# Kernel tuning notes

Hardware: AMD Instinct MI355X
Metric: run time of the kernel (lower is better)

Reference implementation:

```python
import jax, jax.numpy as jnp
import numpy as np

N, E, D_IN, D_H, G = 20000, 320000, 512, 256, 128


def setup_inputs() -> dict:
    key = jax.random.key(0)
    ks = jax.random.split(key, 9)
    x = jax.random.normal(ks[0], (N, D_IN), dtype=jnp.float32)
    edge_index = jax.random.randint(ks[1], (2, E), 0, N, dtype=jnp.int32)
    batch = jnp.sort(jax.random.randint(ks[2], (N,), 0, G, dtype=jnp.int32))
    W1 = jax.random.normal(ks[3], (D_IN, D_H), dtype=jnp.float32) / np.float32(np.sqrt(D_IN))
    b1 = jnp.zeros((D_H,), dtype=jnp.float32)
    W2 = jax.random.normal(ks[4], (D_H, D_H), dtype=jnp.float32) / np.float32(np.sqrt(D_H))
    b2 = jnp.zeros((D_H,), dtype=jnp.float32)
    w_fc = jax.random.normal(ks[5], (D_H, 1), dtype=jnp.float32) / np.float32(np.sqrt(D_H))
    b_fc = jnp.zeros((1,), dtype=jnp.float32)
    return {"x": x, "edge_index": edge_index, "batch": batch,
            "W1": W1, "b1": b1, "W2": W2, "b2": b2, "w_fc": w_fc, "b_fc": b_fc}


def gcn_conv(x, W, b, src, dst, n):
    # PyG GCNConv: out = D^{-1/2} (A+I) D^{-1/2} (X W) + b  (self-loops already in src/dst)
    xw = x @ W                                            # [n, d_out]
    deg = jnp.zeros((n,), xw.dtype).at[dst].add(1.0)       # in-degree incl. self loop
    dinv = jnp.where(deg > 0, jax.lax.rsqrt(deg), 0.0)
    coef = (dinv[src] * dinv[dst])[:, None]               # [e, 1]
    out = jnp.zeros_like(xw).at[dst].add(xw[src] * coef)  # gather-scale-scatter
    return out + b


def reference(x, edge_index, batch, W1, b1, W2, b2, w_fc, b_fc):
    n = x.shape[0]
    loops = jnp.arange(n, dtype=edge_index.dtype)
    src = jnp.concatenate([edge_index[0], loops])
    dst = jnp.concatenate([edge_index[1], loops])
    h = jax.nn.relu(gcn_conv(x, W1, b1, src, dst, n))
    h = jax.nn.relu(gcn_conv(h, W2, b2, src, dst, n))
    # global_mean_pool over graph ids
    sums = jax.ops.segment_sum(h, batch, num_segments=G)                      # [G, d]
    cnt = jax.ops.segment_sum(jnp.ones((n, 1), h.dtype), batch, num_segments=G)
    pooled = sums / jnp.maximum(cnt, 1.0)
    return (pooled @ w_fc + b_fc)[:, 0]                                       # [G]
```

## Files before the change

kernel.cpp:

```cpp
#include <hip/hip_runtime.h>
#include <hip/hip_fp16.h>


#define TPB 256
#define CAP 64

typedef _Float16 hfrag __attribute__((ext_vector_type(8)));
typedef float f32x4 __attribute__((ext_vector_type(4)));
typedef float f32x2 __attribute__((ext_vector_type(2)));

__global__ __launch_bounds__(TPB) void k_init(int* __restrict__ cursor, int N,
                                              const float* __restrict__ W1,
                                              unsigned short* __restrict__ B1, int K1) {
  int nbz = (N + TPB - 1) / TPB;
  int b = blockIdx.x;
  if (b < nbz) {
    int i = b * TPB + threadIdx.x;
    if (i < N) cursor[i] = 0;
    return;
  }
  int t = (b - nbz) * TPB + threadIdx.x;
  if (t >= K1 * 256) return;
  int n = t & 255, k = t >> 8;
  __half h = __float2half(W1[(size_t)k * 256 + n]);
  B1[((size_t)(k >> 5) * 256 + n) * 32 + (k & 31)] = *(unsigned short*)&h;
}

#define LDSTR 72

template <int MODE>
__device__ __forceinline__ void gemm_core(const unsigned short* __restrict__ Bp,
                                          unsigned char* __restrict__ C, int M, int K,
                                          int bm, int bn,
                                          unsigned short (*As)[LDSTR],
                                          const float* A_f32,
                                          const __half* A_f16) {
  const int tid = threadIdx.x;
  const int w = tid >> 6;
  const int lane = tid & 63;
  const int q = lane >> 4;
  const int nin = lane & 15;
  const int r  = tid >> 2;
  const int cb = (tid & 3) << 4;
  const int row = bm + r;
  const bool rok = row < M;

  size_t bbase[2];
#pragma unroll
  for (int nt = 0; nt < 2; ++nt)
    bbase[nt] = ((size_t)(bn + w * 32 + nt * 16 + nin)) * 32 + q * 8;

  f32x4 acc[4][2];
#pragma unroll
  for (int mt = 0; mt < 4; ++mt)
#pragma unroll
    for (int nt = 0; nt < 2; ++nt) acc[mt][nt] = (f32x4){0.f, 0.f, 0.f, 0.f};

  float4 rA[4], rB[4];
  uint4  hA[2], hB[2];

  auto loadf = [&](float4* rf, int kb2) {
    const float* Ap = A_f32 + (size_t)row * K + kb2 + cb;
    rf[0] = *(const float4*)(Ap);
    rf[1] = *(const float4*)(Ap + 4);
    rf[2] = *(const float4*)(Ap + 8);
    rf[3] = *(const float4*)(Ap + 12);
  };
  auto loadh = [&](uint4* rh, int kb2) {
    const __half* Ap = A_f16 + (size_t)row * K + kb2 + cb;
    rh[0] = *(const uint4*)(Ap);
    rh[1] = *(const uint4*)(Ap + 8);
  };
  auto stagef = [&](float4* rf) {
    float vv[16];
    *(float4*)&vv[0] = rf[0]; *(float4*)&vv[4] = rf[1];
    *(float4*)&vv[8] = rf[2]; *(float4*)&vv[12] = rf[3];
    unsigned short h16[16];
#pragma unroll
    for (int j = 0; j < 16; ++j) {
      __half h = __float2half(vv[j]);
      h16[j] = *(unsigned short*)&h;
    }
    __syncthreads();
    *(uint4*)&As[r][cb]     = *(uint4*)&h16[0];
    *(uint4*)&As[r][cb + 8] = *(uint4*)&h16[8];
    __syncthreads();
  };
  auto stageh = [&](uint4* rh) {
    __syncthreads();
    *(uint4*)&As[r][cb]     = rh[0];
    *(uint4*)&As[r][cb + 8] = rh[1];
    __syncthreads();
  };
  auto mfma_step = [&](int kb2) {
#pragma unroll
    for (int s = 0; s < 2; ++s) {
      const size_t koff = (size_t)((kb2 >> 5) + s) * 256 * 32;
      hfrag bf[2];
#pragma unroll
      for (int nt = 0; nt < 2; ++nt)
        bf[nt] = *(const hfrag*)(Bp + koff + bbase[nt]);
      hfrag af[4];
#pragma unroll
      for (int mt = 0; mt < 4; ++mt)
        af[mt] = *(const hfrag*)&As[mt * 16 + nin][s * 32 + q * 8];
#pragma unroll
      for (int mt = 0; mt < 4; ++mt)
#pragma unroll
        for (int nt = 0; nt < 2; ++nt)
          acc[mt][nt] = __builtin_amdgcn_mfma_f32_16x16x32_f16(af[mt], bf[nt], acc[mt][nt], 0, 0, 0);
    }
  };

  if (MODE == 0) {
    rA[0] = make_float4(0.f, 0.f, 0.f, 0.f); rA[1] = rA[0]; rA[2] = rA[0]; rA[3] = rA[0];
    rB[0] = rA[0]; rB[1] = rA[0]; rB[2] = rA[0]; rB[3] = rA[0];
    if (rok) { loadf(rA, 0); loadf(rB, 64); }
  } else {
    hA[0] = make_uint4(0, 0, 0, 0); hA[1] = hA[0];
    hB[0] = hA[0]; hB[1] = hA[0];
    if (rok) { loadh(hA, 0); loadh(hB, 64); }
  }

  for (int kb = 0; kb < K; kb += 128) {
    if (MODE == 0) stagef(rA); else stageh(hA);
    int kpA = kb + 128;
    if (kpA < K && rok) { if (MODE == 0) loadf(rA, kpA); else loadh(hA, kpA); }
    mfma_step(kb);
    if (MODE == 0) stagef(rB); else stageh(hB);
    int kpB = kb + 192;
    if (kpB < K && rok) { if (MODE == 0) loadf(rB, kpB); else loadh(hB, kpB); }
    mfma_step(kb + 64);
  }

#pragma unroll
  for (int mt = 0; mt < 4; ++mt) {
    int rb = bm + mt * 16 + q * 4;
#pragma unroll
    for (int reg = 0; reg < 4; ++reg) {
      int rr = rb + reg;
      if (rr < M) {
#pragma unroll
        for (int nt = 0; nt < 2; ++nt) {
          float v = acc[mt][nt][reg];
          int pk = __builtin_amdgcn_cvt_pk_fp8_f32(v, v, 0, false);
          C[(size_t)rr * 256 + bn + w * 32 + nt * 16 + nin] = (unsigned char)(pk & 0xff);
        }
      }
    }
  }
}

__global__ __launch_bounds__(TPB) void k_gemm1_scatter(const float* __restrict__ A,
                                                       const unsigned short* __restrict__ Bp,
                                                       unsigned char* __restrict__ C, int M, int K,
                                                       const int* __restrict__ src,
                                                       const int* __restrict__ dst,
                                                       int* __restrict__ cursor,
                                                       unsigned* __restrict__ pairw, int E,
                                                       const float* __restrict__ W2,
                                                       unsigned short* __restrict__ W2h) {
  __shared__ unsigned short As[64][LDSTR];
  int nbg = 2 * ((M + 63) / 64);
  int b = blockIdx.x;
  if (b < nbg) {
    gemm_core<0>(Bp, C, M, K, (b >> 1) * 64, (b & 1) * 128, As, A, nullptr);
    return;
  }
  b -= nbg;
  int nbE = (E + TPB - 1) / TPB;
  if (b < nbE) {
    int e = b * TPB + threadIdx.x;
    if (e >= E) return;
    int s = src[e], d = dst[e];
    int pos = d * CAP + atomicAdd(&cursor[d], 1);
    pairw[pos] = (unsigned)s;
    return;
  }
  b -= nbE;
  int t = b * TPB + threadIdx.x;
  if (t >= 256 * 256) return;
  int n = t & 255, k = t >> 8;
  __half h = __float2half(W2[(size_t)k * 256 + n]);
  W2h[((size_t)(k >> 5) * 256 + n) * 32 + (k & 31)] = *(unsigned short*)&h;
}

__global__ __launch_bounds__(TPB) void k_gemm2(const __half* __restrict__ A,
                                               const unsigned short* __restrict__ Bp,
                                               unsigned char* __restrict__ C, int M, int K) {
  __shared__ unsigned short As[64][LDSTR];
  gemm_core<1>(Bp, C, M, K, blockIdx.y * 64, blockIdx.x * 128, As, nullptr, A);
}

__device__ __forceinline__ void fma16(float* a, float coef, uint4 v) {
#pragma unroll
  for (int wv = 0; wv < 4; ++wv) {
    unsigned word = (&v.x)[wv];
    f32x2 lo = __builtin_amdgcn_cvt_pk_f32_fp8((int)word, false);
    f32x2 hi = __builtin_amdgcn_cvt_pk_f32_fp8((int)word, true);
    a[4 * wv + 0] = fmaf(coef, lo[0], a[4 * wv + 0]);
    a[4 * wv + 1] = fmaf(coef, lo[1], a[4 * wv + 1]);
    a[4 * wv + 2] = fmaf(coef, hi[0], a[4 * wv + 2]);
    a[4 * wv + 3] = fmaf(coef, hi[1], a[4 * wv + 3]);
  }
}

__device__ __forceinline__ void gather_loop(float* a, const uint4* __restrict__ xq,
                                            unsigned wreg, int deg, int quarter, int li) {
  int iters = (deg + 3) >> 2;
  int itersP = (iters + 3) & ~3;
  for (int p = 0; p < itersP; p += 4) {
    int k0 = 4 * p + quarter;
    unsigned w0 = (unsigned)__shfl((int)wreg, k0);
    unsigned w1 = (unsigned)__shfl((int)wreg, k0 + 4);
    unsigned w2 = (unsigned)__shfl((int)wreg, k0 + 8);
    unsigned w3 = (unsigned)__shfl((int)wreg, k0 + 12);
    uint4 v0 = xq[((size_t)(w0 >> 16) << 4) + li];
    uint4 v1 = xq[((size_t)(w1 >> 16) << 4) + li];
    uint4 v2 = xq[((size_t)(w2 >> 16) << 4) + li];
    uint4 v3 = xq[((size_t)(w3 >> 16) << 4) + li];
    unsigned short c0 = (unsigned short)(w0 & 0xFFFFu);
    unsigned short c1 = (unsigned short)(w1 & 0xFFFFu);
    unsigned short c2 = (unsigned short)(w2 & 0xFFFFu);
    unsigned short c3 = (unsigned short)(w3 & 0xFFFFu);
    fma16(a, __half2float(*(__half*)&c0), v0);
    fma16(a, __half2float(*(__half*)&c1), v1);
    fma16(a, __half2float(*(__half*)&c2), v2);
    fma16(a, __half2float(*(__half*)&c3), v3);
  }
#pragma unroll
  for (int i = 0; i < 16; ++i) a[i] += __shfl_xor(a[i], 16);
#pragma unroll
  for (int i = 0; i < 16; ++i) a[i] += __shfl_xor(a[i], 32);
}

__global__ __launch_bounds__(TPB) void k_gather1(const uint4* __restrict__ xq,
                                                 const int* __restrict__ cnt,
                                                 unsigned* __restrict__ pairw,
                                                 const float* __restrict__ bias,
                                                 uint4* __restrict__ h1, int N) {
  int node = __builtin_amdgcn_readfirstlane(blockIdx.x * 4 + (threadIdx.x >> 6));
  if (node >= N) return;
  int deg = __builtin_amdgcn_readfirstlane(cnt[node]);
  int lane = threadIdx.x & 63;
  int quarter = lane >> 4, li = lane & 15;
  int base = node * CAP;
  float ci = (float)(deg + 1);

  unsigned wreg = 0u;
  if (lane < deg) {
    int j = (int)pairw[base + lane];
    float c = rsqrtf(ci * (float)(cnt[j] + 1));
    __half hc = __float2half(c);
    wreg = ((unsigned)j << 16) | (unsigned)(*(unsigned short*)&hc);
    pairw[base + lane] = wreg;
  }

  float a[16];
#pragma unroll
  for (int i = 0; i < 16; ++i) a[i] = 0.f;
  gather_loop(a, xq, wreg, deg, quarter, li);

  float di2 = 1.f / ci;
  fma16(a, di2, xq[((size_t)node << 4) + li]);
  if (quarter == 0) {
    const float4 b0 = *(const float4*)&bias[16 * li];
    const float4 b1v = *(const float4*)&bias[16 * li + 4];
    const float4 b2v = *(const float4*)&bias[16 * li + 8];
    const float4 b3v = *(const float4*)&bias[16 * li + 12];
    float r[16];
    r[0] = fmaxf(a[0] + b0.x, 0.f);  r[1] = fmaxf(a[1] + b0.y, 0.f);
    r[2] = fmaxf(a[2] + b0.z, 0.f);  r[3] = fmaxf(a[3] + b0.w, 0.f);
    r[4] = fmaxf(a[4] + b1v.x, 0.f); r[5] = fmaxf(a[5] + b1v.y, 0.f);
    r[6] = fmaxf(a[6] + b1v.z, 0.f); r[7] = fmaxf(a[7] + b1v.w, 0.f);
    r[8] = fmaxf(a[8] + b2v.x, 0.f); r[9] = fmaxf(a[9] + b2v.y, 0.f);
    r[10] = fmaxf(a[10] + b2v.z, 0.f); r[11] = fmaxf(a[11] + b2v.w, 0.f);
    r[12] = fmaxf(a[12] + b3v.x, 0.f); r[13] = fmaxf(a[13] + b3v.y, 0.f);
    r[14] = fmaxf(a[14] + b3v.z, 0.f); r[15] = fmaxf(a[15] + b3v.w, 0.f);
    unsigned o[8];
#pragma unroll
    for (int i = 0; i < 8; ++i) {
      __half2 h2 = __floats2half2_rn(r[2 * i], r[2 * i + 1]);
      o[i] = *(unsigned*)&h2;
    }
    uint4 o0 = make_uint4(o[0], o[1], o[2], o[3]);
    uint4 o1 = make_uint4(o[4], o[5], o[6], o[7]);
    h1[(size_t)node * 32 + 2 * li] = o0;
    h1[(size_t)node * 32 + 2 * li + 1] = o1;
  }
}

__global__ __launch_bounds__(TPB) void k_gather2(const uint4* __restrict__ xq,
                                                 const int* __restrict__ cnt,
                                                 const unsigned* __restrict__ pairw,
                                                 const float* __restrict__ bias,
                                                 const float* __restrict__ wfc,
                                                 float* __restrict__ pdot, int N) {
  int node = __builtin_amdgcn_readfirstlane(blockIdx.x * 4 + (threadIdx.x >> 6));
  if (node >= N) return;
  int deg = __builtin_amdgcn_readfirstlane(cnt[node]);
  int lane = threadIdx.x & 63;
  int quarter = lane >> 4, li = lane & 15;
  int base = node * CAP;

  unsigned wreg = (lane < deg) ? pairw[base + lane] : 0u;

  float a[16];
#pragma unroll
  for (int i = 0; i < 16; ++i) a[i] = 0.f;
  gather_loop(a, xq, wreg, deg, quarter, li);

  float di2 = 1.f / (float)(deg + 1);
  fma16(a, di2, xq[((size_t)node << 4) + li]);

  const float4 b0 = *(const float4*)&bias[16 * li];
  const float4 b1v = *(const float4*)&bias[16 * li + 4];
  const float4 b2v = *(const float4*)&bias[16 * li + 8];
  const float4 b3v = *(const float4*)&bias[16 * li + 12];
  const float4 f0 = *(const float4*)&wfc[16 * li];
  const float4 f1 = *(const float4*)&wfc[16 * li + 4];
  const float4 f2 = *(const float4*)&wfc[16 * li + 8];
  const float4 f3 = *(const float4*)&wfc[16 * li + 12];
  float s = fmaxf(a[0] + b0.x, 0.f) * f0.x + fmaxf(a[1] + b0.y, 0.f) * f0.y +
            fmaxf(a[2] + b0.z, 0.f) * f0.z + fmaxf(a[3] + b0.w, 0.f) * f0.w +
            fmaxf(a[4] + b1v.x, 0.f) * f1.x + fmaxf(a[5] + b1v.y, 0.f) * f1.y +
            fmaxf(a[6] + b1v.z, 0.f) * f1.z + fmaxf(a[7] + b1v.w, 0.f) * f1.w +
            fmaxf(a[8] + b2v.x, 0.f) * f2.x + fmaxf(a[9] + b2v.y, 0.f) * f2.y +
            fmaxf(a[10] + b2v.z, 0.f) * f2.z + fmaxf(a[11] + b2v.w, 0.f) * f2.w +
            fmaxf(a[12] + b3v.x, 0.f) * f3.x + fmaxf(a[13] + b3v.y, 0.f) * f3.y +
            fmaxf(a[14] + b3v.z, 0.f) * f3.z + fmaxf(a[15] + b3v.w, 0.f) * f3.w;
#pragma unroll
  for (int off = 8; off > 0; off >>= 1) s += __shfl_down(s, off, 16);
  if (lane == 0) pdot[node] = s;
}

__global__ __launch_bounds__(TPB) void k_pool(const float* __restrict__ pdot,
                                              const int* __restrict__ batch,
                                              const float* __restrict__ bfc,
                                              float* __restrict__ out, int N) {
  int g = blockIdx.x;
  int lo = 0, hi = N;
  while (lo < hi) { int mid = (lo + hi) >> 1; if (batch[mid] < g) lo = mid + 1; else hi = mid; }
  int start = lo;
  hi = N;
  while (lo < hi) { int mid = (lo + hi) >> 1; if (batch[mid] < g + 1) lo = mid + 1; else hi = mid; }
  int end = lo;

  float s = 0.f;
  for (int i = start + threadIdx.x; i < end; i += TPB) s += pdot[i];
  __shared__ float red[4];
  int lane = threadIdx.x & 63, wave = threadIdx.x >> 6;
#pragma unroll
  for (int off = 32; off > 0; off >>= 1) s += __shfl_down(s, off);
  if (lane == 0) red[wave] = s;
  __syncthreads();
  if (threadIdx.x == 0) {
    float tot = red[0] + red[1] + red[2] + red[3];
    float c = (float)(end - start);
    out[g] = tot / fmaxf(c, 1.f) + bfc[0];
  }
}

extern "C" void kernel_launch(void* const* d_in, const int* in_sizes, int n_in,
                              void* d_out, int out_size, void* d_ws, size_t ws_size,
                              hipStream_t stream) {
  const float* x    = (const float*)d_in[0];
  const int*   eidx = (const int*)d_in[1];
  const int*   batch= (const int*)d_in[2];
  const float* W1   = (const float*)d_in[3];
  const float* b1   = (const float*)d_in[4];
  const float* W2   = (const float*)d_in[5];
  const float* b2   = (const float*)d_in[6];
  const float* wfc  = (const float*)d_in[7];
  const float* bfc  = (const float*)d_in[8];
  float* out = (float*)d_out;

  const int N  = in_sizes[2];
  const int E  = in_sizes[1] / 2;
  const int K1 = in_sizes[0] / N;
  const int G  = out_size;

  const int* srcp = eidx;
  const int* dstp = eidx + E;

  auto al16 = [](size_t v) { return (v + 15) & ~(size_t)15; };
  char* ws = (char*)d_ws;
  size_t off = 0;
  int*      cursor = (int*)(ws + off);         off = al16(off + (size_t)N * 4);
  unsigned* pairw  = (unsigned*)(ws + off);    off = al16(off + (size_t)N * CAP * 4);
  float*    pdot   = (float*)(ws + off);       off = al16(off + (size_t)N * 4);
  unsigned char* bufQ = (unsigned char*)(ws + off); off = al16(off + (size_t)N * 256);
  __half*   h1f    = (__half*)(ws + off);      off = al16(off + (size_t)N * 256 * 2);
  unsigned short* W1h = (unsigned short*)(ws + off); off = al16(off + (size_t)K1 * 256 * 2);
  unsigned short* W2h = (unsigned short*)(ws + off); off = al16(off + (size_t)256 * 256 * 2);

  const int nbz  = (N + TPB - 1) / TPB;
  const int nbW1 = (K1 * 256 + TPB - 1) / TPB;
  const int nbW2 = (256 * 256 + TPB - 1) / TPB;
  const int nbE  = (E + TPB - 1) / TPB;
  const int nbg  = 2 * ((N + 63) / 64);
  const int nbG  = (N + 3) / 4;
  const dim3 g2(2, (N + 63) / 64);

  k_init<<<nbz + nbW1, TPB, 0, stream>>>(cursor, N, W1, W1h, K1);

  k_gemm1_scatter<<<nbg + nbE + nbW2, TPB, 0, stream>>>(x, W1h, bufQ, N, K1,
                                                        srcp, dstp, cursor, pairw, E,
                                                        W2, W2h);
  k_gather1<<<nbG, TPB, 0, stream>>>((const uint4*)bufQ, cursor, pairw, b1,
                                     (uint4*)h1f, N);

  k_gemm2<<<g2, TPB, 0, stream>>>(h1f, W2h, bufQ, N, 256);

  k_gather2<<<nbG, TPB, 0, stream>>>((const uint4*)bufQ, cursor, pairw, b2,
                                     wfc, pdot, N);

  k_pool<<<G, TPB, 0, stream>>>(pdot, batch, bfc, out, N);
}
```

Measured before the change: 169.1 us.

## Drop LDS staging in GEMMs, load MFMA A-fragments directly from global

```diff
diff --git a/kernel.cpp b/kernel.cpp
--- a/kernel.cpp
+++ b/kernel.cpp
@@ -26,125 +26,82 @@
   B1[((size_t)(k >> 5) * 256 + n) * 32 + (k & 31)] = *(unsigned short*)&h;
 }
 
-#define LDSTR 72
-
-template <int MODE>
+template <int AFP32>
 __device__ __forceinline__ void gemm_core(const unsigned short* __restrict__ Bp,
                                           unsigned char* __restrict__ C, int M, int K,
                                           int bm, int bn,
-                                          unsigned short (*As)[LDSTR],
-                                          const float* A_f32,
-                                          const __half* A_f16) {
+                                          const float* __restrict__ A32,
+                                          const __half* __restrict__ A16) {
   const int tid = threadIdx.x;
   const int w = tid >> 6;
   const int lane = tid & 63;
   const int q = lane >> 4;
   const int nin = lane & 15;
-  const int r  = tid >> 2;
-  const int cb = (tid & 3) << 4;
-  const int row = bm + r;
-  const bool rok = row < M;
-
-  size_t bbase[2];
-#pragma unroll
-  for (int nt = 0; nt < 2; ++nt)
-    bbase[nt] = ((size_t)(bn + w * 32 + nt * 16 + nin)) * 32 + q * 8;
-
-  f32x4 acc[4][2];
-#pragma unroll
-  for (int mt = 0; mt < 4; ++mt)
-#pragma unroll
-    for (int nt = 0; nt < 2; ++nt) acc[mt][nt] = (f32x4){0.f, 0.f, 0.f, 0.f};
-
-  float4 rA[4], rB[4];
-  uint4  hA[2], hB[2];
-
-  auto loadf = [&](float4* rf, int kb2) {
-    const float* Ap = A_f32 + (size_t)row * K + kb2 + cb;
-    rf[0] = *(const float4*)(Ap);
-    rf[1] = *(const float4*)(Ap + 4);
-    rf[2] = *(const float4*)(Ap + 8);
-    rf[3] = *(const float4*)(Ap + 12);
-  };
-  auto loadh = [&](uint4* rh, int kb2) {
-    const __half* Ap = A_f16 + (size_t)row * K + kb2 + cb;
-    rh[0] = *(const uint4*)(Ap);
-    rh[1] = *(const uint4*)(Ap + 8);
-  };
-  auto stagef = [&](float4* rf) {
-    float vv[16];
-    *(float4*)&vv[0] = rf[0]; *(float4*)&vv[4] = rf[1];
-    *(float4*)&vv[8] = rf[2]; *(float4*)&vv[12] = rf[3];
-    unsigned short h16[16];
-#pragma unroll
-    for (int j = 0; j < 16; ++j) {
-      __half h = __float2half(vv[j]);
-      h16[j] = *(unsigned short*)&h;
+  const int r0 = bm + w * 32 + nin;
+  const int r1 = r0 + 16;
+  const bool ok0 = r0 < M, ok1 = r1 < M;
+
+  hfrag zf;
+#pragma unroll
+  for (int i = 0; i < 8; ++i) zf[i] = (_Float16)0.f;
+
+  f32x4 acc[2][4];
+#pragma unroll
+  for (int mf = 0; mf < 2; ++mf)
+#pragma unroll
+    for (int nt = 0; nt < 4; ++nt) acc[mf][nt] = (f32x4){0.f, 0.f, 0.f, 0.f};
+
+  const unsigned short* bcol = Bp + (size_t)(bn + nin) * 32 + q * 8;
+
+  for (int kb = 0; kb < K; kb += 32) {
+    hfrag a0 = zf, a1 = zf;
+    if (AFP32) {
+      if (ok0) {
+        const float* p = A32 + (size_t)r0 * K + kb + q * 8;
+        float4 u0 = *(const float4*)p;
+        float4 u1 = *(const float4*)(p + 4);
+        a0[0] = (_Float16)u0.x; a0[1] = (_Float16)u0.y;
+        a0[2] = (_Float16)u0.z; a0[3] = (_Float16)u0.w;
+        a0[4] = (_Float16)u1.x; a0[5] = (_Float16)u1.y;
+        a0[6] = (_Float16)u1.z; a0[7] = (_Float16)u1.w;
+      }
+      if (ok1) {
+        const float* p = A32 + (size_t)r1 * K + kb + q * 8;
+        float4 u0 = *(const float4*)p;
+        float4 u1 = *(const float4*)(p + 4);
+        a1[0] = (_Float16)u0.x; a1[1] = (_Float16)u0.y;
+        a1[2] = (_Float16)u0.z; a1[3] = (_Float16)u0.w;
+        a1[4] = (_Float16)u1.x; a1[5] = (_Float16)u1.y;
+        a1[6] = (_Float16)u1.z; a1[7] = (_Float16)u1.w;
+      }
+    } else {
+      if (ok0) a0 = *(const hfrag*)(A16 + (size_t)r0 * K + kb + q * 8);
+      if (ok1) a1 = *(const hfrag*)(A16 + (size_t)r1 * K + kb + q * 8);
     }
-    __syncthreads();
-    *(uint4*)&As[r][cb]     = *(uint4*)&h16[0];
-    *(uint4*)&As[r][cb + 8] = *(uint4*)&h16[8];
-    __syncthreads();
-  };
-  auto stageh = [&](uint4* rh) {
-    __syncthreads();
-    *(uint4*)&As[r][cb]     = rh[0];
-    *(uint4*)&As[r][cb + 8] = rh[1];
-    __syncthreads();
-  };
-  auto mfma_step = [&](int kb2) {
-#pragma unroll
-    for (int s = 0; s < 2; ++s) {
-      const size_t koff = (size_t)((kb2 >> 5) + s) * 256 * 32;
-      hfrag bf[2];
-#pragma unroll
-      for (int nt = 0; nt < 2; ++nt)
-        bf[nt] = *(const hfrag*)(Bp + koff + bbase[nt]);
-      hfrag af[4];
-#pragma unroll
-      for (int mt = 0; mt < 4; ++mt)
-        af[mt] = *(const hfrag*)&As[mt * 16 + nin][s * 32 + q * 8];
-#pragma unroll
-      for (int mt = 0; mt < 4; ++mt)
-#pragma unroll
-        for (int nt = 0; nt < 2; ++nt)
-          acc[mt][nt] = __builtin_amdgcn_mfma_f32_16x16x32_f16(af[mt], bf[nt], acc[mt][nt], 0, 0, 0);
+    const unsigned short* bk = bcol + (size_t)(kb >> 5) * (256 * 32);
+    hfrag bf[4];
+#pragma unroll
+    for (int nt = 0; nt < 4; ++nt)
+      bf[nt] = *(const hfrag*)(bk + nt * (16 * 32));
+#pragma unroll
+    for (int nt = 0; nt < 4; ++nt) {
+      acc[0][nt] = __builtin_amdgcn_mfma_f32_16x16x32_f16(a0, bf[nt], acc[0][nt], 0, 0, 0);
+      acc[1][nt] = __builtin_amdgcn_mfma_f32_16x16x32_f16(a1, bf[nt], acc[1][nt], 0, 0, 0);
     }
-  };
-
-  if (MODE == 0) {
-    rA[0] = make_float4(0.f, 0.f, 0.f, 0.f); rA[1] = rA[0]; rA[2] = rA[0]; rA[3] = rA[0];
-    rB[0] = rA[0]; rB[1] = rA[0]; rB[2] = rA[0]; rB[3] = rA[0];
-    if (rok) { loadf(rA, 0); loadf(rB, 64); }
-  } else {
-    hA[0] = make_uint4(0, 0, 0, 0); hA[1] = hA[0];
-    hB[0] = hA[0]; hB[1] = hA[0];
-    if (rok) { loadh(hA, 0); loadh(hB, 64); }
-  }
-
-  for (int kb = 0; kb < K; kb += 128) {
-    if (MODE == 0) stagef(rA); else stageh(hA);
-    int kpA = kb + 128;
-    if (kpA < K && rok) { if (MODE == 0) loadf(rA, kpA); else loadh(hA, kpA); }
-    mfma_step(kb);
-    if (MODE == 0) stagef(rB); else stageh(hB);
-    int kpB = kb + 192;
-    if (kpB < K && rok) { if (MODE == 0) loadf(rB, kpB); else loadh(hB, kpB); }
-    mfma_step(kb + 64);
-  }
-
-#pragma unroll
-  for (int mt = 0; mt < 4; ++mt) {
-    int rb = bm + mt * 16 + q * 4;
+  }
+
+#pragma unroll
+  for (int mf = 0; mf < 2; ++mf) {
+    int rb = bm + w * 32 + mf * 16 + q * 4;
 #pragma unroll
     for (int reg = 0; reg < 4; ++reg) {
       int rr = rb + reg;
       if (rr < M) {
 #pragma unroll
-        for (int nt = 0; nt < 2; ++nt) {
-          float v = acc[mt][nt][reg];
+        for (int nt = 0; nt < 4; ++nt) {
+          float v = acc[mf][nt][reg];
           int pk = __builtin_amdgcn_cvt_pk_fp8_f32(v, v, 0, false);
-          C[(size_t)rr * 256 + bn + w * 32 + nt * 16 + nin] = (unsigned char)(pk & 0xff);
+          C[(size_t)rr * 256 + bn + nt * 16 + nin] = (unsigned char)(pk & 0xff);
         }
       }
     }
@@ -160,11 +117,10 @@
                                                        unsigned* __restrict__ pairw, int E,
                                                        const float* __restrict__ W2,
                                                        unsigned short* __restrict__ W2h) {
-  __shared__ unsigned short As[64][LDSTR];
-  int nbg = 2 * ((M + 63) / 64);
+  int nbg = 4 * ((M + 127) / 128);
   int b = blockIdx.x;
   if (b < nbg) {
-    gemm_core<0>(Bp, C, M, K, (b >> 1) * 64, (b & 1) * 128, As, A, nullptr);
+    gemm_core<1>(Bp, C, M, K, (b >> 2) * 128, (b & 3) * 64, A, nullptr);
     return;
   }
   b -= nbg;
@@ -188,8 +144,7 @@
 __global__ __launch_bounds__(TPB) void k_gemm2(const __half* __restrict__ A,
                                                const unsigned short* __restrict__ Bp,
                                                unsigned char* __restrict__ C, int M, int K) {
-  __shared__ unsigned short As[64][LDSTR];
-  gemm_core<1>(Bp, C, M, K, blockIdx.y * 64, blockIdx.x * 128, As, nullptr, A);
+  gemm_core<0>(Bp, C, M, K, blockIdx.y * 128, blockIdx.x * 64, nullptr, A);
 }
 
 __device__ __forceinline__ void fma16(float* a, float coef, uint4 v) {
@@ -398,9 +353,9 @@
   const int nbW1 = (K1 * 256 + TPB - 1) / TPB;
   const int nbW2 = (256 * 256 + TPB - 1) / TPB;
   const int nbE  = (E + TPB - 1) / TPB;
-  const int nbg  = 2 * ((N + 63) / 64);
+  const int nbg  = 4 * ((N + 127) / 128);
   const int nbG  = (N + 3) / 4;
-  const dim3 g2(2, (N + 63) / 64);
+  const dim3 g2(4, (N + 127) / 128);
 
   k_init<<<nbz + nbW1, TPB, 0, stream>>>(cursor, N, W1, W1h, K1);
 
```

Result: slower. 195.3 us (+15.5%).
